# Optimization experiments

Measured on AMD Instinct MI355X. Metric: run time of the kernel, lower is better.

## Reference

```python
import jax, jax.numpy as jnp
import numpy as np

N_NODES = 50000


def _gcn_norm(edge_index, num_nodes):
    # Add self-loops (PyG GCNConv default) and compute symmetric norm.
    loops = jnp.arange(num_nodes, dtype=edge_index.dtype)
    src = jnp.concatenate([edge_index[0], loops])
    dst = jnp.concatenate([edge_index[1], loops])
    ones = jnp.ones(src.shape[0], dtype=jnp.float32)
    deg = jax.ops.segment_sum(ones, dst, num_segments=num_nodes)
    deg_inv_sqrt = jnp.where(deg > 0, jax.lax.rsqrt(jnp.maximum(deg, 1.0)), 0.0)
    norm = deg_inv_sqrt[src] * deg_inv_sqrt[dst]  # [E + N]
    return src, dst, norm


def _gcn_conv(x, src, dst, norm, W, b, num_nodes):
    xw = x @ W                               # [N, out]
    msg = xw[src] * norm[:, None]            # gather + scale  [E+N, out]
    out = jax.ops.segment_sum(msg, dst, num_segments=num_nodes)  # scatter-add
    return out + b


def setup_inputs() -> dict:
    key = jax.random.key(0)
    ks = jax.random.split(key, 10)
    d_in, d_h, d_out = 64, 64, 8
    n_edges = 800000
    x = jax.random.normal(ks[0], (N_NODES, d_in), dtype=jnp.float32)
    edge_index = jax.random.randint(ks[1], (2, n_edges), 0, N_NODES, dtype=jnp.int64)
    def w(k, fan_in, fan_out):
        return jax.random.normal(k, (fan_in, fan_out), dtype=jnp.float32) * (1.0 / np.sqrt(fan_in))
    return {
        "x": x,
        "edge_index": edge_index,
        "W0": w(ks[2], d_in, d_h), "b0": jnp.zeros((d_h,), jnp.float32),
        "W1": w(ks[3], d_h, d_h), "b1": jnp.zeros((d_h,), jnp.float32),
        "W2": w(ks[4], d_h, d_h), "b2": jnp.zeros((d_h,), jnp.float32),
        "linW": w(ks[5], d_h, d_out), "linb": jnp.zeros((d_out,), jnp.float32),
    }


def reference(x, edge_index, W0, b0, W1, b1, W2, b2, linW, linb):
    num_nodes = x.shape[0]
    src, dst, norm = _gcn_norm(edge_index, num_nodes)
    # 3 GCNConv layers, ReLU; dropout is identity at inference (training=False).
    for W, b in ((W0, b0), (W1, b1), (W2, b2)):
        x = jax.nn.relu(_gcn_conv(x, src, dst, norm, W, b, num_nodes))
    return x @ linW + linb
```

## Files before the change

kernel.cpp:

```cpp
#include <hip/hip_runtime.h>
#include <hip/hip_fp16.h>

#define TPB 256
#define CAP 8192
#define CAPSH 13


__device__ __forceinline__ int ld_idx(const void* p, long long i, int is64) {
    return is64 ? (int)((const long long*)p)[i] : ((const int*)p)[i];
}

__device__ __forceinline__ float4 h4_to_f4(ushort4 v) {
    float4 r;
    r.x = __half2float(__ushort_as_half(v.x));
    r.y = __half2float(__ushort_as_half(v.y));
    r.z = __half2float(__ushort_as_half(v.z));
    r.w = __half2float(__ushort_as_half(v.w));
    return r;
}

__device__ __forceinline__ ushort4 f4_to_h4(float4 v) {
    ushort4 r;
    r.x = __half_as_ushort(__float2half_rn(v.x));
    r.y = __half_as_ushort(__float2half_rn(v.y));
    r.z = __half_as_ushort(__float2half_rn(v.z));
    r.w = __half_as_ushort(__float2half_rn(v.w));
    return r;
}

__global__ __launch_bounds__(TPB) void p3_scatter(const void* ei, long long E,
                                                  int* gcur, int* pairs) {
    __shared__ int cnt[TPB];
    __shared__ int cur2[TPB];
    __shared__ int s_is64;
    int t = threadIdx.x;
    if (t < 64) {
        const unsigned int* w = (const unsigned int*)ei;
        unsigned long long m = __ballot(w[2 * t + 1] != 0u);
        if (t == 0) s_is64 = (m == 0ull) ? 1 : 0;
    }
    cnt[t] = 0;
    __syncthreads();
    const int is64 = s_is64;
    long long chunk = (E + gridDim.x - 1) / gridDim.x;
    long long s0 = (long long)blockIdx.x * chunk;
    long long s1 = (s0 + chunk < E) ? s0 + chunk : E;
    for (long long e = s0 + t; e < s1; e += TPB) {
        int d = ld_idx(ei, E + e, is64);
        atomicAdd(&cnt[d >> 8], 1);
    }
    __syncthreads();
    if (cnt[t]) cur2[t] = (t << CAPSH) + atomicAdd(&gcur[t], cnt[t]);
    __syncthreads();
    for (long long e = s0 + t; e < s1; e += TPB) {
        int sv = ld_idx(ei, e, is64);
        int d  = ld_idx(ei, E + e, is64);
        int pos = atomicAdd(&cur2[d >> 8], 1);
        pairs[pos] = (sv << 8) | (d & 255);
    }
}

__global__ __launch_bounds__(TPB) void p4_fill(const int* __restrict__ pairs,
                                               const int* __restrict__ gcur,
                                               const float* __restrict__ x,
                                               int2* __restrict__ meta,
                                               int* __restrict__ csr,
                                               ushort4* __restrict__ z0, int N) {
    __shared__ int ldeg[TPB];
    __shared__ int ssc[TPB];
    __shared__ int cur[TPB];
    __shared__ float fdis[TPB];
    int t = threadIdx.x;
    int b = blockIdx.x;
    int base = b << CAPSH;
    int ecnt = gcur[b];
    ldeg[t] = 0;
    __syncthreads();
    for (int e = base + t; e < base + ecnt; e += TPB)
        atomicAdd(&ldeg[pairs[e] & 255], 1);
    __syncthreads();
    int dv = ldeg[t];
    ssc[t] = dv;
    __syncthreads();
    for (int off = 1; off < TPB; off <<= 1) {
        int u = 0;
        if (t >= off) u = ssc[t - off];
        __syncthreads();
        ssc[t] += u;
        __syncthreads();
    }
    int o = base + ssc[t] - dv;
    cur[t] = o;
    float dd = rsqrtf((float)(dv + 1));
    fdis[t] = dd;
    int node = (b << 8) + t;
    if (node < N)
        meta[node] = make_int2((o << 10) | dv, __float_as_int(dd));
    __syncthreads();
    for (int e = base + t; e < base + ecnt; e += TPB) {
        int p = pairs[e];
        int pos = atomicAdd(&cur[p & 255], 1);
        csr[pos] = p >> 8;
    }

    int ni = t >> 4, c = t & 15;
    for (int p = 0; p < 16; ++p) {
        int nd = (b << 8) + p * 16 + ni;
        if (nd < N) {
            float dvv = fdis[p * 16 + ni];
            float4 h = ((const float4*)x)[nd * 16 + c];
            float4 r = {h.x * dvv, h.y * dvv, h.z * dvv, h.w * dvv};
            z0[nd * 16 + c] = f4_to_h4(r);
        }
    }
}

__device__ __forceinline__ float4 gather_rows(const ushort4* __restrict__ y4,
                                              const int* __restrict__ csr,
                                              int start, int cnt, int c,
                                              float4 acc) {
    const int base = threadIdx.x & 48;
    int j = 0;
    while (j + 16 <= cnt) {
        int idx = csr[start + j + c];
        #pragma unroll
        for (int k = 0; k < 16; ++k) {
            int s = __shfl(idx, base + k);
            float4 v = h4_to_f4(y4[s * 16 + c]);
            acc.x += v.x; acc.y += v.y; acc.z += v.z; acc.w += v.w;
        }
        j += 16;
    }
    int rem = cnt - j;
    if (rem > 0) {
        int idx = (c < rem) ? csr[start + j + c] : 0;
        #pragma unroll
        for (int k = 0; k < 15; ++k) {
            if (k < rem) {
                int s = __shfl(idx, base + k);
                float4 v = h4_to_f4(y4[s * 16 + c]);
                acc.x += v.x; acc.y += v.y; acc.z += v.z; acc.w += v.w;
            }
        }
    }
    return acc;
}

__global__ __launch_bounds__(TPB) void layer_mm(const ushort4* __restrict__ z,
                                                const int* __restrict__ csr,
                                                const int2* __restrict__ meta,
                                                const float* __restrict__ b,
                                                const float* __restrict__ W,
                                                ushort4* __restrict__ zout, int n) {
    __shared__ float Ws[64 * 64];
    __shared__ float hs[16][68];
    int t = threadIdx.x;
    float4* Ws4 = (float4*)Ws;
    const float4* W4g = (const float4*)W;
    #pragma unroll
    for (int i = 0; i < 4; ++i) Ws4[t + i * TPB] = W4g[t + i * TPB];

    int ni = t >> 4, c = t & 15;
    int node = blockIdx.x * 16 + ni;
    float4 s = {0.f, 0.f, 0.f, 0.f};
    float dv = 0.f;
    if (node < n) {
        int2 m = meta[node];
        int start = ((unsigned)m.x) >> 10;
        int cnt = m.x & 1023;
        dv = __int_as_float(m.y);
        s = h4_to_f4(z[node * 16 + c]);
        s = gather_rows(z, csr, start, cnt, c, s);
    }
    __syncthreads();
    *(float4*)&hs[ni][c * 4] = s;
    float4 u = {0.f, 0.f, 0.f, 0.f};
    #pragma unroll
    for (int k = 0; k < 64; ++k) {
        float hv = hs[ni][k];
        float4 w = Ws4[k * 16 + c];
        u.x = fmaf(hv, w.x, u.x);
        u.y = fmaf(hv, w.y, u.y);
        u.z = fmaf(hv, w.z, u.z);
        u.w = fmaf(hv, w.w, u.w);
    }
    if (node < n) {
        float4 bb = ((const float4*)b)[c];
        float4 r;
        r.x = fmaxf(fmaf(dv, u.x, bb.x), 0.f) * dv;
        r.y = fmaxf(fmaf(dv, u.y, bb.y), 0.f) * dv;
        r.z = fmaxf(fmaf(dv, u.z, bb.z), 0.f) * dv;
        r.w = fmaxf(fmaf(dv, u.w, bb.w), 0.f) * dv;
        zout[node * 16 + c] = f4_to_h4(r);
    }
}

__global__ __launch_bounds__(TPB) void layer_final(const ushort4* __restrict__ z,
                                                   const int* __restrict__ csr,
                                                   const int2* __restrict__ meta,
                                                   const float* __restrict__ b,
                                                   const float* __restrict__ W,
                                                   const float* __restrict__ Wl,
                                                   const float* __restrict__ bl,
                                                   float* __restrict__ out, int n) {
    __shared__ float Ws[64 * 64];
    __shared__ float Wls[64 * 8];
    __shared__ float bls[8];
    __shared__ float hs[16][68];
    int t = threadIdx.x;
    float4* Ws4 = (float4*)Ws;
    const float4* W4g = (const float4*)W;
    #pragma unroll
    for (int i = 0; i < 4; ++i) Ws4[t + i * TPB] = W4g[t + i * TPB];
    if (t < 128) ((float4*)Wls)[t] = ((const float4*)Wl)[t];
    if (t < 8) bls[t] = bl[t];

    int ni = t >> 4, c = t & 15;
    int node = blockIdx.x * 16 + ni;
    float4 s = {0.f, 0.f, 0.f, 0.f};
    float dv = 0.f;
    if (node < n) {
        int2 m = meta[node];
        int start = ((unsigned)m.x) >> 10;
        int cnt = m.x & 1023;
        dv = __int_as_float(m.y);
        s = h4_to_f4(z[node * 16 + c]);
        s = gather_rows(z, csr, start, cnt, c, s);
    }
    __syncthreads();
    *(float4*)&hs[ni][c * 4] = s;
    float4 u = {0.f, 0.f, 0.f, 0.f};
    #pragma unroll
    for (int k = 0; k < 64; ++k) {
        float hv = hs[ni][k];
        float4 w = Ws4[k * 16 + c];
        u.x = fmaf(hv, w.x, u.x);
        u.y = fmaf(hv, w.y, u.y);
        u.z = fmaf(hv, w.z, u.z);
        u.w = fmaf(hv, w.w, u.w);
    }
    float4 bb = ((const float4*)b)[c];
    float4 h4;
    h4.x = fmaxf(fmaf(dv, u.x, bb.x), 0.f);
    h4.y = fmaxf(fmaf(dv, u.y, bb.y), 0.f);
    h4.z = fmaxf(fmaf(dv, u.z, bb.z), 0.f);
    h4.w = fmaxf(fmaf(dv, u.w, bb.w), 0.f);
    *(float4*)&hs[ni][c * 4] = h4;
    if (c < 8 && node < n) {
        float acc = bls[c];
        #pragma unroll
        for (int k = 0; k < 64; ++k)
            acc = fmaf(hs[ni][k], Wls[k * 8 + c], acc);
        out[node * 8 + c] = acc;
    }
}

extern "C" void kernel_launch(void* const* d_in, const int* in_sizes, int n_in,
                              void* d_out, int out_size, void* d_ws, size_t ws_size,
                              hipStream_t stream) {
    const float* x  = (const float*)d_in[0];
    const void*  ei = d_in[1];
    const float* W0 = (const float*)d_in[2];
    const float* b0 = (const float*)d_in[3];
    const float* W1 = (const float*)d_in[4];
    const float* b1 = (const float*)d_in[5];
    const float* W2 = (const float*)d_in[6];
    const float* b2 = (const float*)d_in[7];
    const float* Wl = (const float*)d_in[8];
    const float* bl = (const float*)d_in[9];

    const long long E = in_sizes[1] / 2;
    const int dh = in_sizes[3];
    const int din = in_sizes[2] / dh;
    const int N = in_sizes[0] / din;
    const int nb = (N + 255) >> 8;

    char* ws = (char*)d_ws;
    size_t off = 0;
    auto alloc = [&](size_t bytes) -> char* {
        char* r = ws + off;
        off += (bytes + 255) & ~(size_t)255;
        return r;
    };
    int*     gcur    = (int*)    alloc(1024);
    int2*    meta    = (int2*)   alloc((size_t)N * 8);
    int*     pairs   = (int*)    alloc((size_t)nb * CAP * 4);
    int*     csr     = (int*)    alloc((size_t)nb * CAP * 4);
    ushort4* zbA     = (ushort4*)alloc((size_t)N * 64 * 2);
    ushort4* zbB     = (ushort4*)alloc((size_t)N * 64 * 2);

    hipMemsetAsync(gcur, 0, 256 * sizeof(int), stream);
    p3_scatter<<<256, TPB, 0, stream>>>(ei, E, gcur, pairs);
    p4_fill<<<nb, TPB, 0, stream>>>(pairs, gcur, x, meta, csr, zbA, N);

    const int gL = (N + 15) / 16;
    layer_mm<<<gL, TPB, 0, stream>>>(zbA, csr, meta, b0, W0, zbB, N);
    layer_mm<<<gL, TPB, 0, stream>>>(zbB, csr, meta, b1, W1, zbA, N);
    layer_final<<<gL, TPB, 0, stream>>>(zbA, csr, meta, b2, W2, Wl, bl,
                                        (float*)d_out, N);
}
```

Measured before the change: 216.2 us.

## Pad CSR rows to multiples of 16 with zero sentinel and use shuffle-based matmul

Each node's CSR neighbour list is padded up to a multiple of 16 entries. The padding points at a zero sentinel row appended at index N of each feature buffer, which removes the remainder loop in the gather. The per-bucket capacity doubles to hold the padding, and the meta encoding changes to store batch counts. The dense 64x64 and final 64x8 products now broadcast activations with warp shuffles instead of staging them through shared memory. The cost is extra wasted gathers of the zero row and more csr/pairs memory.

```diff
diff --git a/kernel.cpp b/kernel.cpp
--- a/kernel.cpp
+++ b/kernel.cpp
@@ -2,8 +2,8 @@
 #include <hip/hip_fp16.h>
 
 #define TPB 256
-#define CAP 8192
-#define CAPSH 13
+#define CAP 16384
+#define CAPSH 14
 
 
 __device__ __forceinline__ int ld_idx(const void* p, long long i, int is64) {
@@ -80,7 +80,8 @@
         atomicAdd(&ldeg[pairs[e] & 255], 1);
     __syncthreads();
     int dv = ldeg[t];
-    ssc[t] = dv;
+    int pv = (dv + 15) & ~15;
+    ssc[t] = pv;
     __syncthreads();
     for (int off = 1; off < TPB; off <<= 1) {
         int u = 0;
@@ -89,19 +90,20 @@
         ssc[t] += u;
         __syncthreads();
     }
-    int o = base + ssc[t] - dv;
+    int o = base + ssc[t] - pv;
     cur[t] = o;
     float dd = rsqrtf((float)(dv + 1));
     fdis[t] = dd;
     int node = (b << 8) + t;
     if (node < N)
-        meta[node] = make_int2((o << 10) | dv, __float_as_int(dd));
+        meta[node] = make_int2((o << 7) | (pv >> 4), __float_as_int(dd));
     __syncthreads();
     for (int e = base + t; e < base + ecnt; e += TPB) {
         int p = pairs[e];
         int pos = atomicAdd(&cur[p & 255], 1);
         csr[pos] = p >> 8;
     }
+    for (int e = o + dv; e < o + pv; ++e) csr[e] = N;
 
     int ni = t >> 4, c = t & 15;
     for (int p = 0; p < 16; ++p) {
@@ -113,37 +115,43 @@
             z0[nd * 16 + c] = f4_to_h4(r);
         }
     }
+    if (b == 0 && t < 16) z0[(size_t)N * 16 + t] = make_ushort4(0, 0, 0, 0);
 }
 
 __device__ __forceinline__ float4 gather_rows(const ushort4* __restrict__ y4,
                                               const int* __restrict__ csr,
-                                              int start, int cnt, int c,
+                                              int start, int nbatch, int c,
                                               float4 acc) {
     const int base = threadIdx.x & 48;
-    int j = 0;
-    while (j + 16 <= cnt) {
-        int idx = csr[start + j + c];
+    for (int bt = 0; bt < nbatch; ++bt) {
+        int idx = csr[start + bt * 16 + c];
         #pragma unroll
         for (int k = 0; k < 16; ++k) {
             int s = __shfl(idx, base + k);
             float4 v = h4_to_f4(y4[s * 16 + c]);
             acc.x += v.x; acc.y += v.y; acc.z += v.z; acc.w += v.w;
         }
-        j += 16;
-    }
-    int rem = cnt - j;
-    if (rem > 0) {
-        int idx = (c < rem) ? csr[start + j + c] : 0;
+    }
+    return acc;
+}
+
+__device__ __forceinline__ float4 shfl_mm(float4 s, const float4* Ws4, int c) {
+    const int base = threadIdx.x & 48;
+    float4 u = {0.f, 0.f, 0.f, 0.f};
+    #pragma unroll
+    for (int r = 0; r < 4; ++r) {
+        float sr = (r == 0) ? s.x : (r == 1) ? s.y : (r == 2) ? s.z : s.w;
         #pragma unroll
-        for (int k = 0; k < 15; ++k) {
-            if (k < rem) {
-                int s = __shfl(idx, base + k);
-                float4 v = h4_to_f4(y4[s * 16 + c]);
-                acc.x += v.x; acc.y += v.y; acc.z += v.z; acc.w += v.w;
-            }
-        }
-    }
-    return acc;
+        for (int q = 0; q < 16; ++q) {
+            float hv = __shfl(sr, base + q);
+            float4 w = Ws4[(q * 4 + r) * 16 + c];
+            u.x = fmaf(hv, w.x, u.x);
+            u.y = fmaf(hv, w.y, u.y);
+            u.z = fmaf(hv, w.z, u.z);
+            u.w = fmaf(hv, w.w, u.w);
+        }
+    }
+    return u;
 }
 
 __global__ __launch_bounds__(TPB) void layer_mm(const ushort4* __restrict__ z,
@@ -153,12 +161,14 @@
                                                 const float* __restrict__ W,
                                                 ushort4* __restrict__ zout, int n) {
     __shared__ float Ws[64 * 64];
-    __shared__ float hs[16][68];
     int t = threadIdx.x;
     float4* Ws4 = (float4*)Ws;
     const float4* W4g = (const float4*)W;
     #pragma unroll
     for (int i = 0; i < 4; ++i) Ws4[t + i * TPB] = W4g[t + i * TPB];
+
+    if (blockIdx.x == 0 && t < 16)
+        zout[(size_t)n * 16 + t] = make_ushort4(0, 0, 0, 0);
 
     int ni = t >> 4, c = t & 15;
     int node = blockIdx.x * 16 + ni;
@@ -166,24 +176,14 @@
     float dv = 0.f;
     if (node < n) {
         int2 m = meta[node];
-        int start = ((unsigned)m.x) >> 10;
-        int cnt = m.x & 1023;
+        int start = ((unsigned)m.x) >> 7;
+        int nbatch = m.x & 127;
         dv = __int_as_float(m.y);
         s = h4_to_f4(z[node * 16 + c]);
-        s = gather_rows(z, csr, start, cnt, c, s);
-    }
-    __syncthreads();
-    *(float4*)&hs[ni][c * 4] = s;
-    float4 u = {0.f, 0.f, 0.f, 0.f};
-    #pragma unroll
-    for (int k = 0; k < 64; ++k) {
-        float hv = hs[ni][k];
-        float4 w = Ws4[k * 16 + c];
-        u.x = fmaf(hv, w.x, u.x);
-        u.y = fmaf(hv, w.y, u.y);
-        u.z = fmaf(hv, w.z, u.z);
-        u.w = fmaf(hv, w.w, u.w);
-    }
+        s = gather_rows(z, csr, start, nbatch, c, s);
+    }
+    __syncthreads();
+    float4 u = shfl_mm(s, Ws4, c);
     if (node < n) {
         float4 bb = ((const float4*)b)[c];
         float4 r;
@@ -206,7 +206,6 @@
     __shared__ float Ws[64 * 64];
     __shared__ float Wls[64 * 8];
     __shared__ float bls[8];
-    __shared__ float hs[16][68];
     int t = threadIdx.x;
     float4* Ws4 = (float4*)Ws;
     const float4* W4g = (const float4*)W;
@@ -221,38 +220,34 @@
     float dv = 0.f;
     if (node < n) {
         int2 m = meta[node];
-        int start = ((unsigned)m.x) >> 10;
-        int cnt = m.x & 1023;
+        int start = ((unsigned)m.x) >> 7;
+        int nbatch = m.x & 127;
         dv = __int_as_float(m.y);
         s = h4_to_f4(z[node * 16 + c]);
-        s = gather_rows(z, csr, start, cnt, c, s);
-    }
-    __syncthreads();
-    *(float4*)&hs[ni][c * 4] = s;
-    float4 u = {0.f, 0.f, 0.f, 0.f};
-    #pragma unroll
-    for (int k = 0; k < 64; ++k) {
-        float hv = hs[ni][k];
-        float4 w = Ws4[k * 16 + c];
-        u.x = fmaf(hv, w.x, u.x);
-        u.y = fmaf(hv, w.y, u.y);
-        u.z = fmaf(hv, w.z, u.z);
-        u.w = fmaf(hv, w.w, u.w);
-    }
+        s = gather_rows(z, csr, start, nbatch, c, s);
+    }
+    __syncthreads();
+    float4 u = shfl_mm(s, Ws4, c);
     float4 bb = ((const float4*)b)[c];
-    float4 h4;
-    h4.x = fmaxf(fmaf(dv, u.x, bb.x), 0.f);
-    h4.y = fmaxf(fmaf(dv, u.y, bb.y), 0.f);
-    h4.z = fmaxf(fmaf(dv, u.z, bb.z), 0.f);
-    h4.w = fmaxf(fmaf(dv, u.w, bb.w), 0.f);
-    *(float4*)&hs[ni][c * 4] = h4;
-    if (c < 8 && node < n) {
-        float acc = bls[c];
+    float4 h;
+    h.x = fmaxf(fmaf(dv, u.x, bb.x), 0.f);
+    h.y = fmaxf(fmaf(dv, u.y, bb.y), 0.f);
+    h.z = fmaxf(fmaf(dv, u.z, bb.z), 0.f);
+    h.w = fmaxf(fmaf(dv, u.w, bb.w), 0.f);
+
+    const int base = threadIdx.x & 48;
+    int col = c & 7;
+    float acc = bls[col];
+    #pragma unroll
+    for (int r = 0; r < 4; ++r) {
+        float hr = (r == 0) ? h.x : (r == 1) ? h.y : (r == 2) ? h.z : h.w;
         #pragma unroll
-        for (int k = 0; k < 64; ++k)
-            acc = fmaf(hs[ni][k], Wls[k * 8 + c], acc);
-        out[node * 8 + c] = acc;
-    }
+        for (int q = 0; q < 16; ++q) {
+            float hv = __shfl(hr, base + q);
+            acc = fmaf(hv, Wls[(q * 4 + r) * 8 + col], acc);
+        }
+    }
+    if (c < 8 && node < n) out[node * 8 + col] = acc;
 }
 
 extern "C" void kernel_launch(void* const* d_in, const int* in_sizes, int n_in,
@@ -286,8 +281,8 @@
     int2*    meta    = (int2*)   alloc((size_t)N * 8);
     int*     pairs   = (int*)    alloc((size_t)nb * CAP * 4);
     int*     csr     = (int*)    alloc((size_t)nb * CAP * 4);
-    ushort4* zbA     = (ushort4*)alloc((size_t)N * 64 * 2);
-    ushort4* zbB     = (ushort4*)alloc((size_t)N * 64 * 2);
+    ushort4* zbA     = (ushort4*)alloc((size_t)(N + 1) * 64 * 2);
+    ushort4* zbB     = (ushort4*)alloc((size_t)(N + 1) * 64 * 2);
 
     hipMemsetAsync(gcur, 0, 256 * sizeof(int), stream);
     p3_scatter<<<256, TPB, 0, stream>>>(ei, E, gcur, pairs);
```

New measurement: 212.3 us. About the same (-1.8%).
